# Kernel tuning notes

Hardware: AMD Instinct MI355X
Metric: run time of the kernel (lower is better)

Reference implementation:

```python
import jax, jax.numpy as jnp
import numpy as np

B, S, D, H, F = 4, 1024, 1024, 16, 4096
DK = D // H
NEG_INF = jnp.float32(-jnp.inf)


def rmsnorm(x, gamma):
    rms = jnp.sqrt(jnp.mean(x * x, axis=-1, keepdims=True))
    return gamma * x / rms


def masked_softmax(cor):
    # softmax over last dim; rows that are entirely -inf produce all-zero rows
    # (matches the original's NaN -> 0 masked_fill).
    m = jnp.max(cor, axis=-1, keepdims=True)
    m_safe = jnp.where(jnp.isneginf(m), 0.0, m)
    e = jnp.exp(cor - m_safe)
    denom = jnp.sum(e, axis=-1, keepdims=True)
    return e / jnp.where(denom == 0.0, 1.0, denom)


def setup_inputs() -> dict:
    key = jax.random.key(0)
    ks = jax.random.split(key, 12)
    inp = {
        'src': jax.random.normal(ks[0], (B, S, D), jnp.float32),
        'src_padding_mask': jax.random.bernoulli(ks[1], 0.1, (B, S)),
        'prev': jax.random.normal(ks[2], (H, B, S, S), jnp.float32),
        'layer_ind': 2,
        'Wq': jax.random.normal(ks[3], (H, D, DK), jnp.float32) * 0.02,
        'Wk': jax.random.normal(ks[4], (H, D, DK), jnp.float32) * 0.02,
        'Wv': jax.random.normal(ks[5], (H, D, DK), jnp.float32) * 0.02,
        'Wproj': jax.random.normal(ks[6], (D, D), jnp.float32) * 0.02,
        'gamma1': jnp.ones((D,), jnp.float32),
        'gamma2': jnp.ones((D,), jnp.float32),
        'W1': jax.random.normal(ks[7], (D, F), jnp.float32) * 0.02,
        'b1': jnp.zeros((F,), jnp.float32),
        'W2': jax.random.normal(ks[8], (F, D), jnp.float32) * 0.02,
        'b2': jnp.zeros((D,), jnp.float32),
    }
    return inp


def reference(src, src_padding_mask, prev, layer_ind, Wq, Wk, Wv, Wproj,
              gamma1, gamma2, W1, b1, W2, b2):
    ln1 = rmsnorm(src, gamma1)                              # [B,S,D]
    q = jnp.einsum('bsd,hdk->hbsk', ln1, Wq)                # [H,B,S,DK]
    k = jnp.einsum('bsd,hdk->hbsk', ln1, Wk)
    v = jnp.einsum('bsd,hdk->hbsk', ln1, Wv)
    scores = jnp.einsum('hbsk,hbtk->hbst', q, k) * (DK ** -0.5)  # [H,B,S,S]
    qmask = src_padding_mask[None, :, :, None]              # query (row) pad mask
    kvmask = src_padding_mask[None, :, None, :]             # key   (col) pad mask
    scores = jnp.where(qmask, NEG_INF, scores)
    scores = jnp.where(kvmask, NEG_INF, scores)
    raw = (scores + prev) / 2                               # RealFormer residual scores
    cor = raw / (1.0 - 0.5 ** layer_ind)
    w = masked_softmax(cor)                                 # [H,B,S,S]
    att = jnp.einsum('hbst,hbtk->bshk', w, v).reshape(B, S, H * DK)
    attention = att @ Wproj + src                           # residual
    h = jax.nn.relu(rmsnorm(attention, gamma2) @ W1 + b1)
    out = attention + (h @ W2 + b2)
    return out, raw
```

## Files before the change

### kernel.cpp

```cpp
#include <hip/hip_runtime.h>
#include <math.h>

#define Bv 4
#define Sv 1024
#define Dv 1024
#define Hv 16
#define Fv 4096
#define DKv 64

#define MASK_SENTINEL (-3.0e38f)

typedef __attribute__((ext_vector_type(8))) short short8v;
typedef __attribute__((ext_vector_type(4))) float float4v;

__device__ inline unsigned short bf16_rne(float x) {
    unsigned int u = __float_as_uint(x);
    unsigned int r = (u + 0x7FFFu + ((u >> 16) & 1u)) >> 16;
    return (unsigned short)r;
}
__device__ inline float bf16_tof(unsigned short h) {
    return __uint_as_float(((unsigned int)h) << 16);
}
__device__ inline void split2(float x, unsigned short& h, unsigned short& l) {
    unsigned short hh = bf16_rne(x);
    h = hh;
    l = bf16_rne(x - bf16_tof(hh));
}

__global__ __launch_bounds__(256) void rmsnorm_split_k(const float* __restrict__ x,
                                                       const float* __restrict__ g,
                                                       unsigned short* __restrict__ yh,
                                                       unsigned short* __restrict__ yl)
{
    const int row = blockIdx.x;
    const int tid = threadIdx.x;
    const float4* xv = reinterpret_cast<const float4*>(x) + (size_t)row * (Dv / 4);
    float4 v = xv[tid];
    float ss = v.x * v.x + v.y * v.y + v.z * v.z + v.w * v.w;
    #pragma unroll
    for (int o = 32; o > 0; o >>= 1) ss += __shfl_down(ss, o);
    __shared__ float wsum[4];
    if ((tid & 63) == 0) wsum[tid >> 6] = ss;
    __syncthreads();
    const float total = wsum[0] + wsum[1] + wsum[2] + wsum[3];
    const float rinv = rsqrtf(total * (1.0f / Dv));
    const float4 gv = reinterpret_cast<const float4*>(g)[tid];
    float o0 = v.x * gv.x * rinv, o1 = v.y * gv.y * rinv;
    float o2 = v.z * gv.z * rinv, o3 = v.w * gv.w * rinv;
    ushort4 uh, ul; unsigned short h, l;
    split2(o0, h, l); uh.x = h; ul.x = l;
    split2(o1, h, l); uh.y = h; ul.y = l;
    split2(o2, h, l); uh.z = h; ul.z = l;
    split2(o3, h, l); uh.w = h; ul.w = l;
    *(ushort4*)&yh[(size_t)row * Dv + tid * 4] = uh;
    *(ushort4*)&yl[(size_t)row * Dv + tid * 4] = ul;
}

template<bool HEADW>
__global__ __launch_bounds__(256) void tsplit_k(const float* __restrict__ W,
                                                unsigned short* __restrict__ WTh,
                                                unsigned short* __restrict__ WTl,
                                                int K, int N)
{
    __shared__ float tile[64 * 68];
    const int tid = threadIdx.x;
    const int n0 = blockIdx.x * 64, k0 = blockIdx.y * 64;
    #pragma unroll
    for (int it = 0; it < 4; ++it) {
        int slot = it * 256 + tid;
        int r = slot >> 4, c4 = (slot & 15) * 4;
        const float* src;
        if (HEADW)
            src = &W[((size_t)(n0 >> 6) * K + (k0 + r)) * 64 + c4];
        else
            src = &W[(size_t)(k0 + r) * N + n0 + c4];
        *(float4*)&tile[r * 68 + c4] = *(const float4*)src;
    }
    __syncthreads();
    #pragma unroll
    for (int it = 0; it < 4; ++it) {
        int slot = it * 256 + tid;
        int rr = slot >> 4, c4 = (slot & 15) * 4;
        ushort4 uh, ul;
        unsigned short h, l;
        split2(tile[(c4 + 0) * 68 + rr], h, l); uh.x = h; ul.x = l;
        split2(tile[(c4 + 1) * 68 + rr], h, l); uh.y = h; ul.y = l;
        split2(tile[(c4 + 2) * 68 + rr], h, l); uh.z = h; ul.z = l;
        split2(tile[(c4 + 3) * 68 + rr], h, l); uh.w = h; ul.w = l;
        size_t o = (size_t)(n0 + rr) * K + k0 + c4;
        *(ushort4*)&WTh[o] = uh;
        *(ushort4*)&WTl[o] = ul;
    }
}

#define BKP 40
template<int OUTM, bool RELU, bool BIAS, bool RES>
__global__ __launch_bounds__(512) void gemm_mfma_s(const unsigned short* __restrict__ Ahg,
                                                   const unsigned short* __restrict__ Alg,
                                                   const unsigned short* __restrict__ Bhg,
                                                   const unsigned short* __restrict__ Blg,
                                                   const float* __restrict__ bias,
                                                   const float* __restrict__ res,
                                                   float* __restrict__ C,
                                                   unsigned short* __restrict__ Ch,
                                                   unsigned short* __restrict__ Cl,
                                                   int M, int N, int K)
{
    __shared__ unsigned short Ah[128 * BKP], Al[128 * BKP];
    __shared__ unsigned short Bh[128 * BKP], Bl[128 * BKP];
    const int tid = threadIdx.x;
    const int lane = tid & 63, wid = tid >> 6;
    const int wr = wid >> 2, wc = wid & 3;
    const int l15 = lane & 15, lg = lane >> 4;

    const int nx = gridDim.x, ny = gridDim.y;
    const int flat = blockIdx.y * nx + blockIdx.x;
    const int cpx = (nx * ny) >> 3;
    const int g = (flat & 7) * cpx + (flat >> 3);
    const int bn = (g / ny) * 128;
    const int bm = (g % ny) * 128;

    float4v acc[4][2];
    #pragma unroll
    for (int i = 0; i < 4; ++i)
        #pragma unroll
        for (int j = 0; j < 2; ++j) acc[i][j] = (float4v)(0.0f);

    const int sr = tid >> 2, sc8 = (tid & 3) * 8;

    for (int k0 = 0; k0 < K; k0 += 32) {
        *(uint4*)&Ah[sr * BKP + sc8] = *(const uint4*)&Ahg[(size_t)(bm + sr) * K + k0 + sc8];
        *(uint4*)&Al[sr * BKP + sc8] = *(const uint4*)&Alg[(size_t)(bm + sr) * K + k0 + sc8];
        *(uint4*)&Bh[sr * BKP + sc8] = *(const uint4*)&Bhg[(size_t)(bn + sr) * K + k0 + sc8];
        *(uint4*)&Bl[sr * BKP + sc8] = *(const uint4*)&Blg[(size_t)(bn + sr) * K + k0 + sc8];
        __syncthreads();

        short8v fah[4], fal[4], fbh[2], fbl[2];
        const int kb = lg * 8;
        #pragma unroll
        for (int mi = 0; mi < 4; ++mi) {
            int row = wr * 64 + mi * 16 + l15;
            fah[mi] = *(const short8v*)&Ah[row * BKP + kb];
            fal[mi] = *(const short8v*)&Al[row * BKP + kb];
        }
        #pragma unroll
        for (int ni = 0; ni < 2; ++ni) {
            int row = wc * 32 + ni * 16 + l15;
            fbh[ni] = *(const short8v*)&Bh[row * BKP + kb];
            fbl[ni] = *(const short8v*)&Bl[row * BKP + kb];
        }
        #pragma unroll
        for (int mi = 0; mi < 4; ++mi)
            #pragma unroll
            for (int ni = 0; ni < 2; ++ni) {
                float4v c = acc[mi][ni];
                c = __builtin_amdgcn_mfma_f32_16x16x32_bf16(fah[mi], fbh[ni], c, 0, 0, 0);
                c = __builtin_amdgcn_mfma_f32_16x16x32_bf16(fah[mi], fbl[ni], c, 0, 0, 0);
                c = __builtin_amdgcn_mfma_f32_16x16x32_bf16(fal[mi], fbh[ni], c, 0, 0, 0);
                acc[mi][ni] = c;
            }
        __syncthreads();
    }

    #pragma unroll
    for (int mi = 0; mi < 4; ++mi) {
        #pragma unroll
        for (int r = 0; r < 4; ++r) {
            int m = bm + wr * 64 + mi * 16 + lg * 4 + r;
            #pragma unroll
            for (int ni = 0; ni < 2; ++ni) {
                int n = bn + wc * 32 + ni * 16 + l15;
                float v = acc[mi][ni][r];
                if (BIAS) v += bias[n];
                if (RELU) v = fmaxf(v, 0.0f);
                if (RES)  v += res[(size_t)m * N + n];
                if (OUTM == 0) {
                    C[(size_t)m * N + n] = v;
                } else if (OUTM == 1) {
                    unsigned short hi, lo;
                    split2(v, hi, lo);
                    Ch[(size_t)m * N + n] = hi;
                    Cl[(size_t)m * N + n] = lo;
                } else {
                    int hh = n >> 6, dk = n & 63, bb = m >> 10, s = m & 1023;
                    size_t off = (((size_t)(hh * Bv + bb)) * Sv + s) * DKv + dk;
                    unsigned short hi, lo;
                    split2(v, hi, lo);
                    Ch[off] = hi;
                    Cl[off] = lo;
                }
            }
        }
    }
}

__global__ __launch_bounds__(256) void scores_mfma_k(const unsigned short* __restrict__ qh,
                                                     const unsigned short* __restrict__ ql,
                                                     const unsigned short* __restrict__ kh,
                                                     const unsigned short* __restrict__ kl,
                                                     const float* __restrict__ prev,
                                                     const unsigned char* __restrict__ mask,
                                                     const int* __restrict__ layer_ind,
                                                     float* __restrict__ raw,
                                                     float* __restrict__ stat_m,
                                                     float* __restrict__ stat_s)
{
    __shared__ float T[4][16 * 68];
    const int tid = threadIdx.x;
    const int lane = tid & 63, wid = tid >> 6;
    const int wr = wid >> 1, wc = wid & 1;
    const int l15 = lane & 15, lg = lane >> 4;
    const int hb = blockIdx.y, b = hb & 3;
    const int sm = (blockIdx.x >> 3) * 128;
    const int tn = (blockIdx.x & 7) * 128;
    const float cs = 1.0f / (1.0f - exp2f(-(float)layer_ind[0]));

    float4v acc[4][4];
    #pragma unroll
    for (int i = 0; i < 4; ++i)
        #pragma unroll
        for (int j = 0; j < 4; ++j) acc[i][j] = (float4v)(0.0f);

    const size_t qbase = ((size_t)hb * Sv + sm + wr * 64) * DKv;
    const size_t kbase = ((size_t)hb * Sv + tn + wc * 64) * DKv;

    #pragma unroll
    for (int kk = 0; kk < 2; ++kk) {
        const int kb = kk * 32 + lg * 8;
        short8v fah[4], fal[4], fbh[4], fbl[4];
        #pragma unroll
        for (int mi = 0; mi < 4; ++mi) {
            size_t off = qbase + (size_t)(mi * 16 + l15) * DKv + kb;
            fah[mi] = *(const short8v*)&qh[off];
            fal[mi] = *(const short8v*)&ql[off];
        }
        #pragma unroll
        for (int ni = 0; ni < 4; ++ni) {
            size_t off = kbase + (size_t)(ni * 16 + l15) * DKv + kb;
            fbh[ni] = *(const short8v*)&kh[off];
            fbl[ni] = *(const short8v*)&kl[off];
        }
        #pragma unroll
        for (int mi = 0; mi < 4; ++mi)
            #pragma unroll
            for (int ni = 0; ni < 4; ++ni) {
                float4v c = acc[mi][ni];
                c = __builtin_amdgcn_mfma_f32_16x16x32_bf16(fah[mi], fbh[ni], c, 0, 0, 0);
                c = __builtin_amdgcn_mfma_f32_16x16x32_bf16(fah[mi], fbl[ni], c, 0, 0, 0);
                c = __builtin_amdgcn_mfma_f32_16x16x32_bf16(fal[mi], fbh[ni], c, 0, 0, 0);
                acc[mi][ni] = c;
            }
    }

    const int tb2 = (blockIdx.x & 7) * 2 + wc;

    #pragma unroll
    for (int mi = 0; mi < 4; ++mi) {
        #pragma unroll
        for (int ni = 0; ni < 4; ++ni)
            #pragma unroll
            for (int r = 0; r < 4; ++r)
                T[wid][(lg * 4 + r) * 68 + ni * 16 + l15] = acc[mi][ni][r];
        __syncthreads();

        const int s = sm + wr * 64 + mi * 16 + l15;
        const bool qm = mask[b * Sv + s] != 0;
        float xv[16];
        #pragma unroll
        for (int c = 0; c < 4; ++c) {
            float4 tv = *(const float4*)&T[wid][l15 * 68 + lg * 16 + c * 4];
            const int t = tn + wc * 64 + lg * 16 + c * 4;
            const size_t off = ((size_t)hb * Sv + s) * Sv + t;
            const float4 pv = *(const float4*)&prev[off];
            const uchar4 km = *(const uchar4*)&mask[b * Sv + t];
            float4 o;
            o.x = (qm || km.x) ? MASK_SENTINEL : (tv.x * 0.125f + pv.x) * 0.5f;
            o.y = (qm || km.y) ? MASK_SENTINEL : (tv.y * 0.125f + pv.y) * 0.5f;
            o.z = (qm || km.z) ? MASK_SENTINEL : (tv.z * 0.125f + pv.z) * 0.5f;
            o.w = (qm || km.w) ? MASK_SENTINEL : (tv.w * 0.125f + pv.w) * 0.5f;
            *(float4*)&raw[off] = o;
            xv[c * 4 + 0] = (qm || km.x) ? -INFINITY : o.x * cs;
            xv[c * 4 + 1] = (qm || km.y) ? -INFINITY : o.y * cs;
            xv[c * 4 + 2] = (qm || km.z) ? -INFINITY : o.z * cs;
            xv[c * 4 + 3] = (qm || km.w) ? -INFINITY : o.w * cs;
        }
        __syncthreads();

        float mx = -INFINITY;
        #pragma unroll
        for (int j = 0; j < 16; ++j) mx = fmaxf(mx, xv[j]);
        mx = fmaxf(mx, __shfl_xor(mx, 16));
        mx = fmaxf(mx, __shfl_xor(mx, 32));
        float se = 0.0f;
        #pragma unroll
        for (int j = 0; j < 16; ++j)
            se += (xv[j] == -INFINITY) ? 0.0f : __expf(xv[j] - mx);
        se += __shfl_xor(se, 16);
        se += __shfl_xor(se, 32);
        if (lg == 0) {
            const size_t slot = (((size_t)hb * Sv + s) << 4) + tb2;
            stat_m[slot] = mx;
            stat_s[slot] = se;
        }
    }
}

__global__ __launch_bounds__(256) void softmax_pv_k(const float* __restrict__ raw,
                                                    const float* __restrict__ v2d,
                                                    const float* __restrict__ stat_m,
                                                    const float* __restrict__ stat_s,
                                                    const int* __restrict__ layer_ind,
                                                    unsigned short* __restrict__ att2dh,
                                                    unsigned short* __restrict__ att2dl)
{
    __shared__ float Vt[64 * 68];
    __shared__ float Wt[32 * 68];
    __shared__ float rowM[32], rowR[32];
    const int tid = threadIdx.x;
    const int hb = blockIdx.y, h = hb >> 2, b = hb & 3;
    const int s0 = blockIdx.x * 32;
    const float cs = 1.0f / (1.0f - exp2f(-(float)layer_ind[0]));

    if (tid < 32) {
        const size_t base = ((size_t)hb * Sv + s0 + tid) << 4;
        float m = -INFINITY;
        #pragma unroll
        for (int j = 0; j < 16; ++j) m = fmaxf(m, stat_m[base + j]);
        float ssum = 0.0f;
        #pragma unroll
        for (int j = 0; j < 16; ++j) {
            const float sj = stat_s[base + j];
            const float mj = stat_m[base + j];
            if (sj > 0.0f) ssum += __expf(mj - m) * sj;
        }
        rowM[tid] = (m == -INFINITY) ? 0.0f : m;
        rowR[tid] = (ssum == 0.0f) ? 1.0f : 1.0f / ssum;
    }
    __syncthreads();

    const int dk4 = (tid & 15) * 4;
    const int rp2 = tid >> 4;
    const int r0 = rp2 * 2, r1 = r0 + 1;
    float4 a0 = {0, 0, 0, 0}, a1 = {0, 0, 0, 0};

    const int wrow = tid >> 3, wc8 = (tid & 7) * 8;

    for (int tc = 0; tc < Sv; tc += 64) {
        #pragma unroll
        for (int it = 0; it < 4; ++it) {
            int slot = it * 256 + tid;
            int r = slot >> 4, c4 = (slot & 15) * 4;
            *(float4*)&Vt[r * 68 + c4] =
                *(const float4*)&v2d[((size_t)b * Sv + tc + r) * Dv + h * DKv + c4];
        }
        {
            const float mm = rowM[wrow], rc = rowR[wrow];
            const size_t off = ((size_t)hb * Sv + s0 + wrow) * Sv + tc + wc8;
            const float4 x0 = *(const float4*)&raw[off];
            const float4 x1 = *(const float4*)&raw[off + 4];
            float4 e0, e1;
            e0.x = (x0.x < -1e37f) ? 0.0f : __expf(x0.x * cs - mm) * rc;
            e0.y = (x0.y < -1e37f) ? 0.0f : __expf(x0.y * cs - mm) * rc;
            e0.z = (x0.z < -1e37f) ? 0.0f : __expf(x0.z * cs - mm) * rc;
            e0.w = (x0.w < -1e37f) ? 0.0f : __expf(x0.w * cs - mm) * rc;
            e1.x = (x1.x < -1e37f) ? 0.0f : __expf(x1.x * cs - mm) * rc;
            e1.y = (x1.y < -1e37f) ? 0.0f : __expf(x1.y * cs - mm) * rc;
            e1.z = (x1.z < -1e37f) ? 0.0f : __expf(x1.z * cs - mm) * rc;
            e1.w = (x1.w < -1e37f) ? 0.0f : __expf(x1.w * cs - mm) * rc;
            *(float4*)&Wt[wrow * 68 + wc8] = e0;
            *(float4*)&Wt[wrow * 68 + wc8 + 4] = e1;
        }
        __syncthreads();
        #pragma unroll 4
        for (int tt = 0; tt < 64; ++tt) {
            float4 vv = *(const float4*)&Vt[tt * 68 + dk4];
            float w0 = Wt[r0 * 68 + tt];
            float w1 = Wt[r1 * 68 + tt];
            a0.x = fmaf(w0, vv.x, a0.x); a0.y = fmaf(w0, vv.y, a0.y);
            a0.z = fmaf(w0, vv.z, a0.z); a0.w = fmaf(w0, vv.w, a0.w);
            a1.x = fmaf(w1, vv.x, a1.x); a1.y = fmaf(w1, vv.y, a1.y);
            a1.z = fmaf(w1, vv.z, a1.z); a1.w = fmaf(w1, vv.w, a1.w);
        }
        __syncthreads();
    }
    ushort4 uh, ul; unsigned short hh, ll;
    size_t o0 = ((size_t)b * Sv + s0 + r0) * Dv + h * DKv + dk4;
    size_t o1 = ((size_t)b * Sv + s0 + r1) * Dv + h * DKv + dk4;
    split2(a0.x, hh, ll); uh.x = hh; ul.x = ll;
    split2(a0.y, hh, ll); uh.y = hh; ul.y = ll;
    split2(a0.z, hh, ll); uh.z = hh; ul.z = ll;
    split2(a0.w, hh, ll); uh.w = hh; ul.w = ll;
    *(ushort4*)&att2dh[o0] = uh; *(ushort4*)&att2dl[o0] = ul;
    split2(a1.x, hh, ll); uh.x = hh; ul.x = ll;
    split2(a1.y, hh, ll); uh.y = hh; ul.y = ll;
    split2(a1.z, hh, ll); uh.z = hh; ul.z = ll;
    split2(a1.w, hh, ll); uh.w = hh; ul.w = ll;
    *(ushort4*)&att2dh[o1] = uh; *(ushort4*)&att2dl[o1] = ul;
}

extern "C" void kernel_launch(void* const* d_in, const int* in_sizes, int n_in,
                              void* d_out, int out_size, void* d_ws, size_t ws_size,
                              hipStream_t stream)
{
    const float* src          = (const float*)d_in[0];
    const unsigned char* mask = (const unsigned char*)d_in[1];
    const float* prev         = (const float*)d_in[2];
    const int* layer_ind      = (const int*)d_in[3];
    const float* Wq           = (const float*)d_in[4];
    const float* Wk           = (const float*)d_in[5];
    const float* Wv           = (const float*)d_in[6];
    const float* Wproj        = (const float*)d_in[7];
    const float* gamma1       = (const float*)d_in[8];
    const float* gamma2       = (const float*)d_in[9];
    const float* W1           = (const float*)d_in[10];
    const float* b1           = (const float*)d_in[11];
    const float* W2           = (const float*)d_in[12];
    const float* b2           = (const float*)d_in[13];

    float* out = (float*)d_out;
    float* raw = out + (size_t)Bv * Sv * Dv;

    float* ws = (float*)d_ws;
    unsigned short* S16 = (unsigned short*)d_ws;
    const size_t M1 = 1u << 20;
    unsigned short* WT1h = S16;
    unsigned short* WT1l = S16 + 4 * M1;
    unsigned short* WT2h = S16 + 8 * M1;
    unsigned short* WT2l = S16 + 12 * M1;
    unsigned short* WTqh = S16 + 16 * M1, *WTql = S16 + 17 * M1;
    unsigned short* WTkh = S16 + 18 * M1, *WTkl = S16 + 19 * M1;
    unsigned short* WTvh = S16 + 20 * M1, *WTvl = S16 + 21 * M1;
    unsigned short* WTph = S16 + 22 * M1, *WTpl = S16 + 23 * M1;
    unsigned short* ln2h = S16 + 16 * M1, *ln2l = S16 + 20 * M1;
    float* attn = ws + 12 * M1;
    unsigned short* ln1h = S16 + 32 * M1, *ln1l = S16 + 36 * M1;
    float* stat_m = ws + 16 * M1;
    float* stat_s = ws + 17 * M1;
    unsigned short* qh   = S16 + 40 * M1, *ql   = S16 + 44 * M1;
    unsigned short* kh   = S16 + 48 * M1, *kl   = S16 + 52 * M1;
    float* v2d = ws + 28 * M1;
    unsigned short* at2h = S16 + 40 * M1, *at2l = S16 + 44 * M1;
    unsigned short* hbufh = S16 + 32 * M1;
    unsigned short* hbufl = S16 + 48 * M1;
    (void)in_sizes; (void)n_in; (void)out_size; (void)ws_size;

    tsplit_k<true ><<<dim3(16, 16), 256, 0, stream>>>(Wq,    WTqh, WTql, 1024, 1024);
    tsplit_k<true ><<<dim3(16, 16), 256, 0, stream>>>(Wk,    WTkh, WTkl, 1024, 1024);
    tsplit_k<true ><<<dim3(16, 16), 256, 0, stream>>>(Wv,    WTvh, WTvl, 1024, 1024);
    tsplit_k<false><<<dim3(16, 16), 256, 0, stream>>>(Wproj, WTph, WTpl, 1024, 1024);
    tsplit_k<false><<<dim3(64, 16), 256, 0, stream>>>(W1,    WT1h, WT1l, 1024, 4096);
    tsplit_k<false><<<dim3(16, 64), 256, 0, stream>>>(W2,    WT2h, WT2l, 4096, 1024);

    rmsnorm_split_k<<<4096, 256, 0, stream>>>(src, gamma1, ln1h, ln1l);

    dim3 gN1(8, 32);
    gemm_mfma_s<2, false, false, false><<<gN1, 512, 0, stream>>>(ln1h, ln1l, WTqh, WTql, nullptr, nullptr, nullptr, qh, ql, 4096, 1024, 1024);
    gemm_mfma_s<2, false, false, false><<<gN1, 512, 0, stream>>>(ln1h, ln1l, WTkh, WTkl, nullptr, nullptr, nullptr, kh, kl, 4096, 1024, 1024);
    gemm_mfma_s<0, false, false, false><<<gN1, 512, 0, stream>>>(ln1h, ln1l, WTvh, WTvl, nullptr, nullptr, v2d, nullptr, nullptr, 4096, 1024, 1024);

    scores_mfma_k<<<dim3(64, 64), 256, 0, stream>>>(qh, ql, kh, kl, prev, mask, layer_ind, raw, stat_m, stat_s);

    softmax_pv_k<<<dim3(32, 64), 256, 0, stream>>>(raw, v2d, stat_m, stat_s, layer_ind, at2h, at2l);

    gemm_mfma_s<0, false, false, true><<<gN1, 512, 0, stream>>>(at2h, at2l, WTph, WTpl, nullptr, src, attn, nullptr, nullptr, 4096, 1024, 1024);

    rmsnorm_split_k<<<4096, 256, 0, stream>>>(attn, gamma2, ln2h, ln2l);

    gemm_mfma_s<1, true, true, false><<<dim3(32, 32), 512, 0, stream>>>(ln2h, ln2l, WT1h, WT1l, b1, nullptr, nullptr, hbufh, hbufl, 4096, 4096, 1024);

    gemm_mfma_s<0, false, true, true><<<gN1, 512, 0, stream>>>(hbufh, hbufl, WT2h, WT2l, b2, attn, out, nullptr, nullptr, 4096, 1024, 4096);
}
```

Measured before the change: 989.7 us.

## Fuse QKV projections into one GEMM and switch to 64x128 tiles

The three Q/K/V projection GEMMs become one GEMM with N=3072. Their transposed bf16 hi/lo weights are laid out contiguously, and the epilogue routes each output segment to the q, k (head-major split) or v (fp32) buffer. All GEMMs move to a new kernel with 64x128 block tiles, 256 threads and a plain row-major block order instead of the grouped swizzle. The goal is fewer launches and more blocks per GEMM for better occupancy and wave balance. The cost is less data reuse per tile and possibly worse L2 locality without the swizzle.

```diff
diff --git a/kernel.cpp b/kernel.cpp
--- a/kernel.cpp
+++ b/kernel.cpp
@@ -94,31 +94,26 @@
 }
 
 #define BKP 40
+#define KOFF ((size_t)8 << 20)
 template<int OUTM, bool RELU, bool BIAS, bool RES>
-__global__ __launch_bounds__(512) void gemm_mfma_s(const unsigned short* __restrict__ Ahg,
-                                                   const unsigned short* __restrict__ Alg,
-                                                   const unsigned short* __restrict__ Bhg,
-                                                   const unsigned short* __restrict__ Blg,
-                                                   const float* __restrict__ bias,
-                                                   const float* __restrict__ res,
-                                                   float* __restrict__ C,
-                                                   unsigned short* __restrict__ Ch,
-                                                   unsigned short* __restrict__ Cl,
-                                                   int M, int N, int K)
-{
-    __shared__ unsigned short Ah[128 * BKP], Al[128 * BKP];
+__global__ __launch_bounds__(256) void gemm64(const unsigned short* __restrict__ Ahg,
+                                              const unsigned short* __restrict__ Alg,
+                                              const unsigned short* __restrict__ Bhg,
+                                              const unsigned short* __restrict__ Blg,
+                                              const float* __restrict__ bias,
+                                              const float* __restrict__ res,
+                                              float* __restrict__ C,
+                                              unsigned short* __restrict__ Ch,
+                                              unsigned short* __restrict__ Cl,
+                                              int M, int N, int K)
+{
+    __shared__ unsigned short Ah[64 * BKP], Al[64 * BKP];
     __shared__ unsigned short Bh[128 * BKP], Bl[128 * BKP];
     const int tid = threadIdx.x;
     const int lane = tid & 63, wid = tid >> 6;
-    const int wr = wid >> 2, wc = wid & 3;
+    const int wc = wid;
     const int l15 = lane & 15, lg = lane >> 4;
-
-    const int nx = gridDim.x, ny = gridDim.y;
-    const int flat = blockIdx.y * nx + blockIdx.x;
-    const int cpx = (nx * ny) >> 3;
-    const int g = (flat & 7) * cpx + (flat >> 3);
-    const int bn = (g / ny) * 128;
-    const int bm = (g % ny) * 128;
+    const int bm = blockIdx.y * 64, bn = blockIdx.x * 128;
 
     float4v acc[4][2];
     #pragma unroll
@@ -131,15 +126,20 @@
     for (int k0 = 0; k0 < K; k0 += 32) {
         *(uint4*)&Ah[sr * BKP + sc8] = *(const uint4*)&Ahg[(size_t)(bm + sr) * K + k0 + sc8];
         *(uint4*)&Al[sr * BKP + sc8] = *(const uint4*)&Alg[(size_t)(bm + sr) * K + k0 + sc8];
-        *(uint4*)&Bh[sr * BKP + sc8] = *(const uint4*)&Bhg[(size_t)(bn + sr) * K + k0 + sc8];
-        *(uint4*)&Bl[sr * BKP + sc8] = *(const uint4*)&Blg[(size_t)(bn + sr) * K + k0 + sc8];
+        #pragma unroll
+        for (int it = 0; it < 2; ++it) {
+            int slot = it * 256 + tid;
+            int r = slot >> 2, c8 = (slot & 3) * 8;
+            *(uint4*)&Bh[r * BKP + c8] = *(const uint4*)&Bhg[(size_t)(bn + r) * K + k0 + c8];
+            *(uint4*)&Bl[r * BKP + c8] = *(const uint4*)&Blg[(size_t)(bn + r) * K + k0 + c8];
+        }
         __syncthreads();
 
         short8v fah[4], fal[4], fbh[2], fbl[2];
         const int kb = lg * 8;
         #pragma unroll
         for (int mi = 0; mi < 4; ++mi) {
-            int row = wr * 64 + mi * 16 + l15;
+            int row = mi * 16 + l15;
             fah[mi] = *(const short8v*)&Ah[row * BKP + kb];
             fal[mi] = *(const short8v*)&Al[row * BKP + kb];
         }
@@ -166,7 +166,7 @@
     for (int mi = 0; mi < 4; ++mi) {
         #pragma unroll
         for (int r = 0; r < 4; ++r) {
-            int m = bm + wr * 64 + mi * 16 + lg * 4 + r;
+            int m = bm + mi * 16 + lg * 4 + r;
             #pragma unroll
             for (int ni = 0; ni < 2; ++ni) {
                 int n = bn + wc * 32 + ni * 16 + l15;
@@ -182,12 +182,18 @@
                     Ch[(size_t)m * N + n] = hi;
                     Cl[(size_t)m * N + n] = lo;
                 } else {
-                    int hh = n >> 6, dk = n & 63, bb = m >> 10, s = m & 1023;
-                    size_t off = (((size_t)(hh * Bv + bb)) * Sv + s) * DKv + dk;
-                    unsigned short hi, lo;
-                    split2(v, hi, lo);
-                    Ch[off] = hi;
-                    Cl[off] = lo;
+                    const int seg = n >> 10, nn = n & 1023;
+                    if (seg == 2) {
+                        C[(size_t)m * 1024 + nn] = v;
+                    } else {
+                        const int hh = nn >> 6, dk = nn & 63, bb = m >> 10, s = m & 1023;
+                        size_t off = (((size_t)(hh * Bv + bb)) * Sv + s) * DKv + dk
+                                   + (size_t)seg * KOFF;
+                        unsigned short hi, lo;
+                        split2(v, hi, lo);
+                        Ch[off] = hi;
+                        Cl[off] = lo;
+                    }
                 }
             }
         }
@@ -427,11 +433,10 @@
     unsigned short* WT1l = S16 + 4 * M1;
     unsigned short* WT2h = S16 + 8 * M1;
     unsigned short* WT2l = S16 + 12 * M1;
-    unsigned short* WTqh = S16 + 16 * M1, *WTql = S16 + 17 * M1;
-    unsigned short* WTkh = S16 + 18 * M1, *WTkl = S16 + 19 * M1;
-    unsigned short* WTvh = S16 + 20 * M1, *WTvl = S16 + 21 * M1;
-    unsigned short* WTph = S16 + 22 * M1, *WTpl = S16 + 23 * M1;
-    unsigned short* ln2h = S16 + 16 * M1, *ln2l = S16 + 20 * M1;
+    unsigned short* WTallh = S16 + 16 * M1;
+    unsigned short* WTalll = S16 + 19 * M1;
+    unsigned short* WTph   = S16 + 22 * M1, *WTpl = S16 + 23 * M1;
+    unsigned short* ln2h   = S16 + 16 * M1, *ln2l = S16 + 20 * M1;
     float* attn = ws + 12 * M1;
     unsigned short* ln1h = S16 + 32 * M1, *ln1l = S16 + 36 * M1;
     float* stat_m = ws + 16 * M1;
@@ -444,29 +449,26 @@
     unsigned short* hbufl = S16 + 48 * M1;
     (void)in_sizes; (void)n_in; (void)out_size; (void)ws_size;
 
-    tsplit_k<true ><<<dim3(16, 16), 256, 0, stream>>>(Wq,    WTqh, WTql, 1024, 1024);
-    tsplit_k<true ><<<dim3(16, 16), 256, 0, stream>>>(Wk,    WTkh, WTkl, 1024, 1024);
-    tsplit_k<true ><<<dim3(16, 16), 256, 0, stream>>>(Wv,    WTvh, WTvl, 1024, 1024);
+    tsplit_k<true ><<<dim3(16, 16), 256, 0, stream>>>(Wq,    WTallh,          WTalll,          1024, 1024);
+    tsplit_k<true ><<<dim3(16, 16), 256, 0, stream>>>(Wk,    WTallh + M1,     WTalll + M1,     1024, 1024);
+    tsplit_k<true ><<<dim3(16, 16), 256, 0, stream>>>(Wv,    WTallh + 2 * M1, WTalll + 2 * M1, 1024, 1024);
     tsplit_k<false><<<dim3(16, 16), 256, 0, stream>>>(Wproj, WTph, WTpl, 1024, 1024);
     tsplit_k<false><<<dim3(64, 16), 256, 0, stream>>>(W1,    WT1h, WT1l, 1024, 4096);
     tsplit_k<false><<<dim3(16, 64), 256, 0, stream>>>(W2,    WT2h, WT2l, 4096, 1024);
 
     rmsnorm_split_k<<<4096, 256, 0, stream>>>(src, gamma1, ln1h, ln1l);
 
-    dim3 gN1(8, 32);
-    gemm_mfma_s<2, false, false, false><<<gN1, 512, 0, stream>>>(ln1h, ln1l, WTqh, WTql, nullptr, nullptr, nullptr, qh, ql, 4096, 1024, 1024);
-    gemm_mfma_s<2, false, false, false><<<gN1, 512, 0, stream>>>(ln1h, ln1l, WTkh, WTkl, nullptr, nullptr, nullptr, kh, kl, 4096, 1024, 1024);
-    gemm_mfma_s<0, false, false, false><<<gN1, 512, 0, stream>>>(ln1h, ln1l, WTvh, WTvl, nullptr, nullptr, v2d, nullptr, nullptr, 4096, 1024, 1024);
+    gemm64<3, false, false, false><<<dim3(24, 64), 256, 0, stream>>>(ln1h, ln1l, WTallh, WTalll, nullptr, nullptr, v2d, qh, ql, 4096, 3072, 1024);
 
     scores_mfma_k<<<dim3(64, 64), 256, 0, stream>>>(qh, ql, kh, kl, prev, mask, layer_ind, raw, stat_m, stat_s);
 
     softmax_pv_k<<<dim3(32, 64), 256, 0, stream>>>(raw, v2d, stat_m, stat_s, layer_ind, at2h, at2l);
 
-    gemm_mfma_s<0, false, false, true><<<gN1, 512, 0, stream>>>(at2h, at2l, WTph, WTpl, nullptr, src, attn, nullptr, nullptr, 4096, 1024, 1024);
+    gemm64<0, false, false, true><<<dim3(8, 64), 256, 0, stream>>>(at2h, at2l, WTph, WTpl, nullptr, src, attn, nullptr, nullptr, 4096, 1024, 1024);
 
     rmsnorm_split_k<<<4096, 256, 0, stream>>>(attn, gamma2, ln2h, ln2l);
 
-    gemm_mfma_s<1, true, true, false><<<dim3(32, 32), 512, 0, stream>>>(ln2h, ln2l, WT1h, WT1l, b1, nullptr, nullptr, hbufh, hbufl, 4096, 4096, 1024);
-
-    gemm_mfma_s<0, false, true, true><<<gN1, 512, 0, stream>>>(hbufh, hbufl, WT2h, WT2l, b2, attn, out, nullptr, nullptr, 4096, 1024, 4096);
-}
+    gemm64<1, true, true, false><<<dim3(32, 64), 256, 0, stream>>>(ln2h, ln2l, WT1h, WT1l, b1, nullptr, nullptr, hbufh, hbufl, 4096, 4096, 1024);
+
+    gemm64<0, false, true, true><<<dim3(8, 64), 256, 0, stream>>>(hbufh, hbufl, WT2h, WT2l, b2, attn, out, nullptr, nullptr, 4096, 1024, 4096);
+}
```

After: 831.1 us. 1.19x faster.
